# Kernel optimization log

Measured on AMD Instinct MI355X. Metric: run time of the kernel, lower is better.

Reference implementation:

```python
import jax, jax.numpy as jnp
import numpy as np

B, S, H = 2, 2048, 2048
NH = 16
HD = H // NH  # 128


def setup_inputs() -> dict:
    key = jax.random.key(0)
    ks = jax.random.split(key, 6)
    sc = 0.02
    return {
        "x": jax.random.normal(ks[0], (B, S, H), dtype=jnp.float32),
        "attention_mask": jnp.zeros((B, S), dtype=jnp.float32),
        "Wq": jax.random.normal(ks[1], (H, H), dtype=jnp.float32) * sc,
        "bq": jnp.zeros((H,), dtype=jnp.float32),
        "Wk": jax.random.normal(ks[2], (H, H), dtype=jnp.float32) * sc,
        "bk": jnp.zeros((H,), dtype=jnp.float32),
        "Wv": jax.random.normal(ks[3], (H, H), dtype=jnp.float32) * sc,
        "bv": jnp.zeros((H,), dtype=jnp.float32),
        "Wo": jax.random.normal(ks[4], (H, H), dtype=jnp.float32) * sc,
        "bo": jnp.zeros((H,), dtype=jnp.float32),
    }


def reference(x, attention_mask, Wq, bq, Wk, bk, Wv, bv, Wo, bo):
    b, s, h = x.shape
    q = (x @ Wq + bq).reshape(b, s, NH, HD)
    k = (x @ Wk + bk).reshape(b, s, NH, HD)
    v = (x @ Wv + bv).reshape(b, s, NH, HD)
    scale = 1.0 / jnp.sqrt(jnp.asarray(HD, dtype=x.dtype))
    scores = jnp.einsum('bqhd,bkhd->bhqk', q, k) * scale
    scores = scores + attention_mask[:, None, None, :]
    weights = jax.nn.softmax(scores, axis=-1)
    attn = jnp.einsum('bhqk,bkhd->bqhd', weights, v).reshape(b, s, h)
    return attn @ Wo + bo
```

## Files before the change

### kernel.cpp

```cpp
#include <hip/hip_runtime.h>
#include <hip/hip_bf16.h>
#include <stdint.h>

#define BB   2
#define SS   2048
#define HHH  2048
#define NHH  16
#define HDD  128
#define MTOT 4096

typedef __bf16 bf16x8 __attribute__((ext_vector_type(8)));
typedef float  f32x4  __attribute__((ext_vector_type(4)));
typedef float  f32x16 __attribute__((ext_vector_type(16)));

#define MFMA16(a, b, c) __builtin_amdgcn_mfma_f32_16x16x32_bf16((a), (b), (c), 0, 0, 0)
#define MFMA32(a, b, c) __builtin_amdgcn_mfma_f32_32x32x16_bf16((a), (b), (c), 0, 0, 0)

__device__ __forceinline__ unsigned short f2bf(float f) {
    union { float f; unsigned u; } v; v.f = f;
    unsigned r = v.u + 0x7FFFu + ((v.u >> 16) & 1u);
    return (unsigned short)(r >> 16);
}

__device__ __forceinline__ unsigned packbf(float a, float b) {
    union { __bf16 h[2]; unsigned u; } p;
    p.h[0] = (__bf16)a; p.h[1] = (__bf16)b;
    return p.u;
}

__device__ __forceinline__ void pswap(unsigned &a, unsigned &b) {
    asm("v_permlane32_swap_b32 %0, %1" : "+v"(a), "+v"(b));
}

__device__ __forceinline__ float2 xswap(float x) {
    unsigned a = __builtin_bit_cast(unsigned, x);
    unsigned b;
    asm("v_mov_b32 %0, %1" : "=v"(b) : "v"(a));
    asm("v_permlane32_swap_b32 %0, %1" : "+v"(a), "+v"(b));
    return make_float2(__builtin_bit_cast(float, a), __builtin_bit_cast(float, b));
}

__device__ __forceinline__ void gload16(const void* src, void* lds) {
    __builtin_amdgcn_global_load_lds(
        (__attribute__((address_space(1))) void*)src,
        (__attribute__((address_space(3))) void*)lds,
        16, 0, 0);
}

__global__ void cast_f32_bf16(const float* __restrict__ in,
                              unsigned short* __restrict__ out, int n) {
    int i = (blockIdx.x * blockDim.x + threadIdx.x) * 4;
    int stride = gridDim.x * blockDim.x * 4;
    for (; i < n; i += stride) {
        float4 v = *(const float4*)(in + i);
        ushort4 o;
        o.x = f2bf(v.x); o.y = f2bf(v.y); o.z = f2bf(v.z); o.w = f2bf(v.w);
        *(ushort4*)(out + i) = o;
    }
}

__global__ void scale_mask(const float* __restrict__ in, float* __restrict__ out) {
    int i = blockIdx.x * 256 + threadIdx.x;
    out[i] = in[i] * 1.4426950408889634f;
}

__global__ void transpose_cast4(const float* __restrict__ W0, const float* __restrict__ W1,
                                const float* __restrict__ W2, const float* __restrict__ W3,
                                unsigned short* __restrict__ out) {
    const float* in = blockIdx.z == 0 ? W0 : blockIdx.z == 1 ? W1 : blockIdx.z == 2 ? W2 : W3;
    unsigned short* o = out + (size_t)blockIdx.z * ((size_t)HHH * HHH);
    __shared__ float tile[32][33];
    int c0 = blockIdx.x * 32, r0 = blockIdx.y * 32;
    int tx = threadIdx.x, ty = threadIdx.y;
    #pragma unroll
    for (int i = 0; i < 32; i += 8)
        tile[ty + i][tx] = in[(size_t)(r0 + ty + i) * HHH + c0 + tx];
    __syncthreads();
    #pragma unroll
    for (int i = 0; i < 32; i += 8)
        o[(size_t)(c0 + ty + i) * HHH + r0 + tx] = f2bf(tile[tx][ty + i]);
}

template<int MODE>
__global__ __launch_bounds__(512, 2) void gemm8_bf16(
    const unsigned short* __restrict__ A,
    const unsigned short* __restrict__ Bt,
    const float* __restrict__ bias,
    void* __restrict__ Cout,
    int M, int N, int K)
{
    __shared__ __align__(16) unsigned char sm[147456];
    const int tid = threadIdx.x;
    const int wv = tid >> 6, ln = tid & 63;
    const int g = ln >> 4, r = ln & 15;
    const int wr = wv >> 2, wc = wv & 3;

    const int bid = blockIdx.x;
    const int lb = (bid & 7) * 32 + (bid >> 3);
    const int m0 = (lb & 31) * 128;
    const int n0 = (lb >> 5) * 256;

    unsigned srcA[2]; int ldsA[2];
    #pragma unroll
    for (int j = 0; j < 2; ++j) {
        int o = j * 8192 + tid * 16;
        int row = o >> 7;
        int lg = ((o >> 4) & 7) ^ (row & 7);
        srcA[j] = (unsigned)(m0 + row) * K + lg * 8;
        ldsA[j] = o;
    }
    unsigned srcB[4]; int ldsB[4];
    #pragma unroll
    for (int j = 0; j < 4; ++j) {
        int o = j * 8192 + tid * 16;
        int row = o >> 7;
        int lg = ((o >> 4) & 7) ^ (row & 7);
        srcB[j] = (unsigned)(n0 + row) * K + lg * 8;
        ldsB[j] = 16384 + o;
    }

    f32x4 acc[4][4];
    #pragma unroll
    for (int i = 0; i < 4; ++i)
        #pragma unroll
        for (int j = 0; j < 4; ++j)
            acc[i][j] = (f32x4){0.f, 0.f, 0.f, 0.f};

    const int NT = K >> 6;

    {
        unsigned char* b0 = sm;
        unsigned char* b1 = sm + 49152;
        #pragma unroll
        for (int j = 0; j < 2; ++j) gload16(A + srcA[j], b0 + ldsA[j]);
        #pragma unroll
        for (int j = 0; j < 4; ++j) gload16(Bt + srcB[j], b0 + ldsB[j]);
        #pragma unroll
        for (int j = 0; j < 2; ++j) gload16(A + srcA[j] + 64, b1 + ldsA[j]);
        #pragma unroll
        for (int j = 0; j < 4; ++j) gload16(Bt + srcB[j] + 64, b1 + ldsB[j]);
    }
    asm volatile("s_waitcnt vmcnt(6)" ::: "memory");
    __builtin_amdgcn_s_barrier();

    int csel = 0;
    int psel = 2;
    for (int t = 0; t < NT; ++t) {
        const unsigned char* Ab = sm + csel * 49152;
        const unsigned char* Bb = Ab + 16384;
        unsigned char* Pb = sm + psel * 49152;
        const bool pre = (t + 2 < NT);
        const int ko = (t + 2) * 64;

        bf16x8 af[2][2], bfr[4][2];
        #define LDA(mi, ks) (*(const bf16x8*)(Ab + (wr * 64 + (mi) * 16 + r) * 128 + \
                             ((((ks) << 2) + g) ^ ((wr * 64 + (mi) * 16 + r) & 7)) * 16))
        #define LDB(ni, ks) (*(const bf16x8*)(Bb + (wc * 64 + (ni) * 16 + r) * 128 + \
                             ((((ks) << 2) + g) ^ ((wc * 64 + (ni) * 16 + r) & 7)) * 16))

        af[0][0] = LDA(0, 0); af[0][1] = LDA(0, 1);
        af[1][0] = LDA(1, 0); af[1][1] = LDA(1, 1);
        #pragma unroll
        for (int ni = 0; ni < 4; ++ni) {
            bfr[ni][0] = LDB(ni, 0);
            bfr[ni][1] = LDB(ni, 1);
        }
        if (pre) { gload16(Bt + srcB[0] + ko, Pb + ldsB[0]);
                   gload16(Bt + srcB[1] + ko, Pb + ldsB[1]);
                   gload16(Bt + srcB[2] + ko, Pb + ldsB[2]); }
        __builtin_amdgcn_s_barrier();
        asm volatile("s_waitcnt lgkmcnt(0)" ::: "memory");
        __builtin_amdgcn_s_setprio(1);
        #pragma unroll
        for (int mi = 0; mi < 2; ++mi)
            #pragma unroll
            for (int ni = 0; ni < 4; ++ni)
                #pragma unroll
                for (int ks = 0; ks < 2; ++ks)
                    acc[mi][ni] = MFMA16(af[mi][ks], bfr[ni][ks], acc[mi][ni]);
        __builtin_amdgcn_s_setprio(0);
        __builtin_amdgcn_s_barrier();

        af[0][0] = LDA(2, 0); af[0][1] = LDA(2, 1);
        af[1][0] = LDA(3, 0); af[1][1] = LDA(3, 1);
        if (pre) { gload16(Bt + srcB[3] + ko, Pb + ldsB[3]);
                   gload16(A + srcA[0] + ko, Pb + ldsA[0]);
                   gload16(A + srcA[1] + ko, Pb + ldsA[1]); }
        __builtin_amdgcn_s_barrier();
        asm volatile("s_waitcnt lgkmcnt(0)" ::: "memory");
        __builtin_amdgcn_s_setprio(1);
        #pragma unroll
        for (int mi = 0; mi < 2; ++mi)
            #pragma unroll
            for (int ni = 0; ni < 4; ++ni)
                #pragma unroll
                for (int ks = 0; ks < 2; ++ks)
                    acc[mi + 2][ni] = MFMA16(af[mi][ks], bfr[ni][ks], acc[mi + 2][ni]);
        __builtin_amdgcn_s_setprio(0);

        if (pre) asm volatile("s_waitcnt vmcnt(6)" ::: "memory");
        else     asm volatile("s_waitcnt vmcnt(0)" ::: "memory");
        __builtin_amdgcn_s_barrier();

        csel = (csel == 2) ? 0 : csel + 1;
        psel = (psel == 2) ? 0 : psel + 1;
        #undef LDA
        #undef LDB
    }

    #pragma unroll
    for (int mt = 0; mt < 4; ++mt) {
        #pragma unroll
        for (int nt = 0; nt < 4; ++nt) {
            int col = n0 + wc * 64 + nt * 16 + r;
            float bvv = bias[col];
            f32x4 a = acc[mt][nt];
            int mrow = m0 + wr * 64 + mt * 16 + g * 4;
            if (MODE == 0) {
                #pragma unroll
                for (int q = 0; q < 4; ++q)
                    ((unsigned short*)Cout)[(size_t)(mrow + q) * N + col] = f2bf(a[q] + bvv);
            } else if (MODE == 2) {
                #pragma unroll
                for (int q = 0; q < 4; ++q)
                    ((float*)Cout)[(size_t)(mrow + q) * N + col] = a[q] + bvv;
            } else {
                int b = mrow >> 11, s0x = mrow & 2047;
                ushort4 o;
                o.x = f2bf(a[0] + bvv); o.y = f2bf(a[1] + bvv);
                o.z = f2bf(a[2] + bvv); o.w = f2bf(a[3] + bvv);
                *(ushort4*)((unsigned short*)Cout + ((size_t)(b * 2048 + col)) * 2048 + s0x) = o;
            }
        }
    }
}

__global__ __launch_bounds__(256, 2) void attn_fwd(
    const unsigned short* __restrict__ Q,
    const unsigned short* __restrict__ K,
    const unsigned short* __restrict__ V,
    const float* __restrict__ maskl2,
    unsigned short* __restrict__ O)
{
    __shared__ __align__(16) unsigned char sm[57344];
    const int tid = threadIdx.x, wv = tid >> 6, ln = tid & 63;
    const int hi = ln >> 5, qr = ln & 31;

    const int bid = blockIdx.x;
    const int lb = (bid & 7) * 64 + (bid >> 3);
    const int qb = lb & 15;
    const int bh = lb >> 4;
    const int h = bh & 15, b = bh >> 4;

    const size_t rowQ0 = (size_t)(b * 2048 + qb * 128 + wv * 32);
    const float SCL2 = 0.08838834764831845f * 1.4426950408889634f;

    unsigned srcK[2], srcV[2];
    int ldsK[2], ldsV[2];
    #pragma unroll
    for (int i = 0; i < 2; ++i) {
        int ch = wv * 2 + i;
        int o = ch * 1024 + ln * 16;
        { int row = o >> 8; int gl = ((o >> 4) & 15) ^ (row & 7);
          srcK[i] = (unsigned)((b * 2048 + row) * 2048 + h * 128 + gl * 8);
          ldsK[i] = o; }
        { int d = o >> 6; int gl = ((o >> 4) & 3) ^ ((d >> 1) & 3);
          srcV[i] = (unsigned)((b * 2048 + h * 128 + d) * 2048 + gl * 8);
          ldsV[i] = 8192 + o; }
    }

    #define STAGE(t, base) { \
        _Pragma("unroll") \
        for (int i = 0; i < 2; ++i) { \
            gload16(K + srcK[i] + (unsigned)(t) * (32u * 2048u), sm + (base) + ldsK[i]); \
            gload16(V + srcV[i] + (unsigned)(t) * 32u, sm + (base) + ldsV[i]); \
        } }

    #pragma unroll
    for (int i = 0; i < 2; ++i)
        gload16(maskl2 + b * 2048 + wv * 512 + i * 256 + ln * 4,
                sm + 49152 + wv * 2048 + i * 1024);
    STAGE(0, 0); STAGE(1, 16384); STAGE(2, 32768);

    bf16x8 qf[8];
    #pragma unroll
    for (int ks = 0; ks < 8; ++ks)
        qf[ks] = *(const bf16x8*)(Q + (rowQ0 + qr) * 2048 + h * 128 + ks * 16 + hi * 8);

    f32x16 acc[4];
    #pragma unroll
    for (int i = 0; i < 4; ++i)
        #pragma unroll
        for (int j = 0; j < 16; ++j)
            acc[i][j] = 0.f;
    float mr = -3.0e38f, lr = 0.f;

    const float* ml = (const float*)(sm + 49152);

    asm volatile("s_waitcnt vmcnt(8)" ::: "memory");
    __builtin_amdgcn_s_barrier();

    int bufo = 0;
    for (int t = 0; t < 64; ++t) {
        const unsigned char* Kt = sm + bufo;
        const unsigned char* Vt = Kt + 8192;

        f32x4 mk[4];
        #pragma unroll
        for (int rg = 0; rg < 4; ++rg)
            mk[rg] = *(const f32x4*)(ml + t * 32 + rg * 8 + hi * 4);

        f32x16 sfA, sfB;
        #pragma unroll
        for (int j = 0; j < 16; ++j) { sfA[j] = 0.f; sfB[j] = 0.f; }
        __builtin_amdgcn_s_setprio(1);
        #pragma unroll
        for (int ks = 0; ks < 4; ++ks) {
            int s0 = (2 * ks + hi) ^ (qr & 7);
            bf16x8 kf = *(const bf16x8*)(Kt + qr * 256 + s0 * 16);
            sfA = MFMA32(kf, qf[ks], sfA);
        }
        #pragma unroll
        for (int ks = 4; ks < 8; ++ks) {
            int s0 = (2 * ks + hi) ^ (qr & 7);
            bf16x8 kf = *(const bf16x8*)(Kt + qr * 256 + s0 * 16);
            sfB = MFMA32(kf, qf[ks], sfB);
        }
        __builtin_amdgcn_s_setprio(0);

        float sv[16];
        #pragma unroll
        for (int reg = 0; reg < 16; ++reg)
            sv[reg] = (sfA[reg] + sfB[reg]) * SCL2 + mk[reg >> 2][reg & 3];

        float mx[8];
        #pragma unroll
        for (int j = 0; j < 8; ++j)
            mx[j] = fmaxf(sv[2 * j], sv[2 * j + 1]);
        float m01 = fmaxf(fmaxf(fmaxf(mx[0], mx[1]), fmaxf(mx[2], mx[3])),
                          fmaxf(fmaxf(mx[4], mx[5]), fmaxf(mx[6], mx[7])));
        float2 mp = xswap(m01);
        float mt = fmaxf(mp.x, mp.y);

        float alpha = 1.f;
        int allskip = __all(mt <= mr + 8.f);
        if (!allskip) {
            float nm = fmaxf(mr, mt);
            alpha = __builtin_amdgcn_exp2f(mr - nm);
            mr = nm;
            #pragma unroll
            for (int dblk = 0; dblk < 4; ++dblk)
                #pragma unroll
                for (int reg = 0; reg < 16; ++reg)
                    acc[dblk][reg] *= alpha;
        }

        float s0 = 0.f, s1 = 0.f, s2 = 0.f, s3 = 0.f;
        #pragma unroll
        for (int reg = 0; reg < 16; reg += 4) {
            float p0 = __builtin_amdgcn_exp2f(sv[reg + 0] - mr);
            float p1 = __builtin_amdgcn_exp2f(sv[reg + 1] - mr);
            float p2 = __builtin_amdgcn_exp2f(sv[reg + 2] - mr);
            float p3 = __builtin_amdgcn_exp2f(sv[reg + 3] - mr);
            sv[reg + 0] = p0; sv[reg + 1] = p1;
            sv[reg + 2] = p2; sv[reg + 3] = p3;
            s0 += p0; s1 += p1; s2 += p2; s3 += p3;
        }
        float rsl = (s0 + s1) + (s2 + s3);
        float2 rp = xswap(rsl);
        float rs = rp.x + rp.y;
        lr = lr * alpha + rs;

        bf16x8 pfr[2];
        #pragma unroll
        for (int kb16 = 0; kb16 < 2; ++kb16) {
            unsigned W00 = packbf(sv[(2*kb16+0)*4 + 0], sv[(2*kb16+0)*4 + 1]);
            unsigned W01 = packbf(sv[(2*kb16+0)*4 + 2], sv[(2*kb16+0)*4 + 3]);
            unsigned W10 = packbf(sv[(2*kb16+1)*4 + 0], sv[(2*kb16+1)*4 + 1]);
            unsigned W11 = packbf(sv[(2*kb16+1)*4 + 2], sv[(2*kb16+1)*4 + 3]);
            pswap(W00, W10);
            pswap(W01, W11);
            union { unsigned w[4]; bf16x8 v; } u;
            u.w[0] = W00; u.w[1] = W01; u.w[2] = W10; u.w[3] = W11;
            pfr[kb16] = u.v;
        }

        __builtin_amdgcn_s_setprio(1);
        #pragma unroll
        for (int dblk = 0; dblk < 4; ++dblk) {
            int d = dblk * 32 + qr;
            f32x16 a = acc[dblk];
            #pragma unroll
            for (int kb16 = 0; kb16 < 2; ++kb16) {
                int s = (2 * kb16 + hi) ^ ((d >> 1) & 3);
                bf16x8 vf = *(const bf16x8*)(Vt + d * 64 + s * 16);
                a = MFMA32(vf, pfr[kb16], a);
            }
            acc[dblk] = a;
        }
        __builtin_amdgcn_s_setprio(0);

        asm volatile("s_waitcnt vmcnt(4)" ::: "memory");
        __builtin_amdgcn_s_barrier();

        if (t + 3 < 64) STAGE(t + 3, bufo);
        bufo = (bufo == 32768) ? 0 : bufo + 16384;
    }

    float linv = 1.f / lr;
    unsigned short* orow = O + (rowQ0 + qr) * 2048 + h * 128;
    #pragma unroll
    for (int dblk = 0; dblk < 4; ++dblk)
        #pragma unroll
        for (int rg = 0; rg < 4; ++rg) {
            float v0 = acc[dblk][rg * 4 + 0] * linv;
            float v1 = acc[dblk][rg * 4 + 1] * linv;
            float v2 = acc[dblk][rg * 4 + 2] * linv;
            float v3 = acc[dblk][rg * 4 + 3] * linv;
            uint2 o;
            o.x = packbf(v0, v1);
            o.y = packbf(v2, v3);
            *(uint2*)(orow + dblk * 32 + rg * 8 + hi * 4) = o;
        }
    #undef STAGE
}

extern "C" void kernel_launch(void* const* d_in, const int* in_sizes, int n_in,
                              void* d_out, int out_size, void* d_ws, size_t ws_size,
                              hipStream_t stream)
{
    (void)in_sizes; (void)n_in; (void)out_size; (void)ws_size;
    const float* x    = (const float*)d_in[0];
    const float* mask = (const float*)d_in[1];
    const float* Wq   = (const float*)d_in[2];
    const float* bq   = (const float*)d_in[3];
    const float* Wk   = (const float*)d_in[4];
    const float* bk   = (const float*)d_in[5];
    const float* Wv   = (const float*)d_in[6];
    const float* bv   = (const float*)d_in[7];
    const float* Wo   = (const float*)d_in[8];
    const float* bo   = (const float*)d_in[9];
    float* out = (float*)d_out;

    char* ws = (char*)d_ws;
    unsigned short* xb  = (unsigned short*)(ws);
    unsigned short* Wqt = (unsigned short*)(ws + (16u << 20));
    unsigned short* Wkt = (unsigned short*)(ws + (24u << 20));
    unsigned short* Wvt = (unsigned short*)(ws + (32u << 20));
    unsigned short* Wot = (unsigned short*)(ws + (40u << 20));
    unsigned short* Qb  = (unsigned short*)(ws + (48u << 20));
    unsigned short* Kb  = (unsigned short*)(ws + (64u << 20));
    unsigned short* Vtb = (unsigned short*)(ws + (80u << 20));
    unsigned short* Ab  = (unsigned short*)(ws + (16u << 20));
    float*          mkl = (float*)(ws + (32u << 20));

    cast_f32_bf16<<<2048, 256, 0, stream>>>(x, xb, MTOT * HHH);
    transpose_cast4<<<dim3(64, 64, 4), dim3(32, 8), 0, stream>>>(Wq, Wk, Wv, Wo, Wqt);

    gemm8_bf16<0><<<256, 512, 0, stream>>>(xb, Wqt, bq, Qb,  MTOT, HHH, HHH);
    gemm8_bf16<0><<<256, 512, 0, stream>>>(xb, Wkt, bk, Kb,  MTOT, HHH, HHH);
    gemm8_bf16<1><<<256, 512, 0, stream>>>(xb, Wvt, bv, Vtb, MTOT, HHH, HHH);

    scale_mask<<<(BB * SS) / 256, 256, 0, stream>>>(mask, mkl);
    attn_fwd<<<512, 256, 0, stream>>>(Qb, Kb, Vtb, mkl, Ab);

    gemm8_bf16<2><<<256, 512, 0, stream>>>(Ab, Wot, bo, out, MTOT, HHH, HHH);
}
```

Measured before the change: 279.6 us.

## Merge QKV projections into one launch and software-pipeline QK^T in attention

The three Q/K/V projection GEMMs are merged into a single 768-block launch over the concatenated transposed weights, with per-region bias and output-layout selection in the epilogue. This removes two launches and fills the GPU better than three 256-block GEMMs would. The attention kernel is restructured so the QK^T scores for the next key tile are computed before the current tile's softmax/PV step, with a peeled prologue and epilogue and adjusted waitcnt/barriers, so score MFMAs overlap the softmax work. The cost is more live registers, an extra barrier per iteration, and more complex synchronisation.

```diff
diff --git a/kernel.cpp b/kernel.cpp
--- a/kernel.cpp
+++ b/kernel.cpp
@@ -81,13 +81,110 @@
         o[(size_t)(c0 + ty + i) * HHH + r0 + tx] = f2bf(tile[tx][ty + i]);
 }
 
-template<int MODE>
-__global__ __launch_bounds__(512, 2) void gemm8_bf16(
+#define GEMM_CORE(A_, Bt_, K_, m0_, n0_)                                              \
+    unsigned srcA[2]; int ldsA[2];                                                    \
+    _Pragma("unroll")                                                                 \
+    for (int j = 0; j < 2; ++j) {                                                     \
+        int o = j * 8192 + tid * 16;                                                  \
+        int row = o >> 7;                                                             \
+        int lg = ((o >> 4) & 7) ^ (row & 7);                                          \
+        srcA[j] = (unsigned)(m0_ + row) * K_ + lg * 8;                                \
+        ldsA[j] = o;                                                                  \
+    }                                                                                 \
+    unsigned srcB[4]; int ldsB[4];                                                    \
+    _Pragma("unroll")                                                                 \
+    for (int j = 0; j < 4; ++j) {                                                     \
+        int o = j * 8192 + tid * 16;                                                  \
+        int row = o >> 7;                                                             \
+        int lg = ((o >> 4) & 7) ^ (row & 7);                                          \
+        srcB[j] = (unsigned)(n0_ + row) * K_ + lg * 8;                                \
+        ldsB[j] = 16384 + o;                                                          \
+    }                                                                                 \
+    f32x4 acc[4][4];                                                                  \
+    _Pragma("unroll")                                                                 \
+    for (int i = 0; i < 4; ++i)                                                       \
+        _Pragma("unroll")                                                             \
+        for (int j = 0; j < 4; ++j)                                                   \
+            acc[i][j] = (f32x4){0.f, 0.f, 0.f, 0.f};                                  \
+    const int NT = K_ >> 6;                                                           \
+    {                                                                                 \
+        unsigned char* b0 = sm;                                                       \
+        unsigned char* b1 = sm + 49152;                                               \
+        _Pragma("unroll")                                                             \
+        for (int j = 0; j < 2; ++j) gload16(A_ + srcA[j], b0 + ldsA[j]);              \
+        _Pragma("unroll")                                                             \
+        for (int j = 0; j < 4; ++j) gload16(Bt_ + srcB[j], b0 + ldsB[j]);             \
+        _Pragma("unroll")                                                             \
+        for (int j = 0; j < 2; ++j) gload16(A_ + srcA[j] + 64, b1 + ldsA[j]);         \
+        _Pragma("unroll")                                                             \
+        for (int j = 0; j < 4; ++j) gload16(Bt_ + srcB[j] + 64, b1 + ldsB[j]);        \
+    }                                                                                 \
+    asm volatile("s_waitcnt vmcnt(6)" ::: "memory");                                  \
+    __builtin_amdgcn_s_barrier();                                                     \
+    int csel = 0, psel = 2;                                                           \
+    for (int t = 0; t < NT; ++t) {                                                    \
+        const unsigned char* Ab = sm + csel * 49152;                                  \
+        const unsigned char* Bb = Ab + 16384;                                         \
+        unsigned char* Pb = sm + psel * 49152;                                        \
+        const bool pre = (t + 2 < NT);                                                \
+        const int ko = (t + 2) * 64;                                                  \
+        bf16x8 af[2][2], bfr[4][2];                                                   \
+        af[0][0] = LDA(0, 0); af[0][1] = LDA(0, 1);                                   \
+        af[1][0] = LDA(1, 0); af[1][1] = LDA(1, 1);                                   \
+        _Pragma("unroll")                                                             \
+        for (int ni = 0; ni < 4; ++ni) { bfr[ni][0] = LDB(ni, 0); bfr[ni][1] = LDB(ni, 1); } \
+        if (pre) { gload16(Bt_ + srcB[0] + ko, Pb + ldsB[0]);                         \
+                   gload16(Bt_ + srcB[1] + ko, Pb + ldsB[1]);                         \
+                   gload16(Bt_ + srcB[2] + ko, Pb + ldsB[2]); }                       \
+        __builtin_amdgcn_s_barrier();                                                 \
+        asm volatile("s_waitcnt lgkmcnt(0)" ::: "memory");                            \
+        __builtin_amdgcn_s_setprio(1);                                                \
+        _Pragma("unroll")                                                             \
+        for (int mi = 0; mi < 2; ++mi)                                                \
+            _Pragma("unroll")                                                         \
+            for (int ni = 0; ni < 4; ++ni)                                            \
+                _Pragma("unroll")                                                     \
+                for (int ks = 0; ks < 2; ++ks)                                        \
+                    acc[mi][ni] = MFMA16(af[mi][ks], bfr[ni][ks], acc[mi][ni]);       \
+        __builtin_amdgcn_s_setprio(0);                                                \
+        __builtin_amdgcn_s_barrier();                                                 \
+        af[0][0] = LDA(2, 0); af[0][1] = LDA(2, 1);                                   \
+        af[1][0] = LDA(3, 0); af[1][1] = LDA(3, 1);                                   \
+        if (pre) { gload16(Bt_ + srcB[3] + ko, Pb + ldsB[3]);                         \
+                   gload16(A_ + srcA[0] + ko, Pb + ldsA[0]);                          \
+                   gload16(A_ + srcA[1] + ko, Pb + ldsA[1]); }                        \
+        __builtin_amdgcn_s_barrier();                                                 \
+        asm volatile("s_waitcnt lgkmcnt(0)" ::: "memory");                            \
+        __builtin_amdgcn_s_setprio(1);                                                \
+        _Pragma("unroll")                                                             \
+        for (int mi = 0; mi < 2; ++mi)                                                \
+            _Pragma("unroll")                                                         \
+            for (int ni = 0; ni < 4; ++ni)                                            \
+                _Pragma("unroll")                                                     \
+                for (int ks = 0; ks < 2; ++ks)                                        \
+                    acc[mi + 2][ni] = MFMA16(af[mi][ks], bfr[ni][ks], acc[mi + 2][ni]); \
+        __builtin_amdgcn_s_setprio(0);                                                \
+        if (pre) asm volatile("s_waitcnt vmcnt(6)" ::: "memory");                     \
+        else     asm volatile("s_waitcnt vmcnt(0)" ::: "memory");                     \
+        __builtin_amdgcn_s_barrier();                                                 \
+        csel = (csel == 2) ? 0 : csel + 1;                                            \
+        psel = (psel == 2) ? 0 : psel + 1;                                            \
+    }
+
+#define LDA(mi, ks) (*(const bf16x8*)(Ab + (wr * 64 + (mi) * 16 + r) * 128 + \
+                     ((((ks) << 2) + g) ^ ((wr * 64 + (mi) * 16 + r) & 7)) * 16))
+#define LDB(ni, ks) (*(const bf16x8*)(Bb + (wc * 64 + (ni) * 16 + r) * 128 + \
+                     ((((ks) << 2) + g) ^ ((wc * 64 + (ni) * 16 + r) & 7)) * 16))
+
+__global__ __launch_bounds__(512, 2) void gemmQKV(
     const unsigned short* __restrict__ A,
     const unsigned short* __restrict__ Bt,
-    const float* __restrict__ bias,
-    void* __restrict__ Cout,
-    int M, int N, int K)
+    const float* __restrict__ bq,
+    const float* __restrict__ bk,
+    const float* __restrict__ bv,
+    unsigned short* __restrict__ Qb,
+    unsigned short* __restrict__ Kb,
+    unsigned short* __restrict__ Vtb)
 {
     __shared__ __align__(16) unsigned char sm[147456];
     const int tid = threadIdx.x;
@@ -96,117 +193,59 @@
     const int wr = wv >> 2, wc = wv & 3;
 
     const int bid = blockIdx.x;
+    const int lb = (bid & 7) * 96 + (bid >> 3);
+    const int m0 = (lb & 31) * 128;
+    const int n0 = (lb >> 5) * 256;
+    const int K = HHH;
+
+    GEMM_CORE(A, Bt, K, m0, n0)
+
+    const int region = n0 >> 11;
+    const float* bp = region == 0 ? bq : (region == 1 ? bk : bv);
+    unsigned short* outp = region == 0 ? Qb : Kb;
+    #pragma unroll
+    for (int mt = 0; mt < 4; ++mt) {
+        #pragma unroll
+        for (int nt = 0; nt < 4; ++nt) {
+            int col = n0 + wc * 64 + nt * 16 + r;
+            int lcol = col & 2047;
+            float bvv = bp[lcol];
+            f32x4 a = acc[mt][nt];
+            int mrow = m0 + wr * 64 + mt * 16 + g * 4;
+            if (region < 2) {
+                #pragma unroll
+                for (int q = 0; q < 4; ++q)
+                    outp[(size_t)(mrow + q) * 2048 + lcol] = f2bf(a[q] + bvv);
+            } else {
+                int b = mrow >> 11, s0x = mrow & 2047;
+                ushort4 o;
+                o.x = f2bf(a[0] + bvv); o.y = f2bf(a[1] + bvv);
+                o.z = f2bf(a[2] + bvv); o.w = f2bf(a[3] + bvv);
+                *(ushort4*)(Vtb + ((size_t)(b * 2048 + lcol)) * 2048 + s0x) = o;
+            }
+        }
+    }
+}
+
+__global__ __launch_bounds__(512, 2) void gemmO(
+    const unsigned short* __restrict__ A,
+    const unsigned short* __restrict__ Bt,
+    const float* __restrict__ bias,
+    float* __restrict__ Cout)
+{
+    __shared__ __align__(16) unsigned char sm[147456];
+    const int tid = threadIdx.x;
+    const int wv = tid >> 6, ln = tid & 63;
+    const int g = ln >> 4, r = ln & 15;
+    const int wr = wv >> 2, wc = wv & 3;
+
+    const int bid = blockIdx.x;
     const int lb = (bid & 7) * 32 + (bid >> 3);
     const int m0 = (lb & 31) * 128;
     const int n0 = (lb >> 5) * 256;
-
-    unsigned srcA[2]; int ldsA[2];
-    #pragma unroll
-    for (int j = 0; j < 2; ++j) {
-        int o = j * 8192 + tid * 16;
-        int row = o >> 7;
-        int lg = ((o >> 4) & 7) ^ (row & 7);
-        srcA[j] = (unsigned)(m0 + row) * K + lg * 8;
-        ldsA[j] = o;
-    }
-    unsigned srcB[4]; int ldsB[4];
-    #pragma unroll
-    for (int j = 0; j < 4; ++j) {
-        int o = j * 8192 + tid * 16;
-        int row = o >> 7;
-        int lg = ((o >> 4) & 7) ^ (row & 7);
-        srcB[j] = (unsigned)(n0 + row) * K + lg * 8;
-        ldsB[j] = 16384 + o;
-    }
-
-    f32x4 acc[4][4];
-    #pragma unroll
-    for (int i = 0; i < 4; ++i)
-        #pragma unroll
-        for (int j = 0; j < 4; ++j)
-            acc[i][j] = (f32x4){0.f, 0.f, 0.f, 0.f};
-
-    const int NT = K >> 6;
-
-    {
-        unsigned char* b0 = sm;
-        unsigned char* b1 = sm + 49152;
-        #pragma unroll
-        for (int j = 0; j < 2; ++j) gload16(A + srcA[j], b0 + ldsA[j]);
-        #pragma unroll
-        for (int j = 0; j < 4; ++j) gload16(Bt + srcB[j], b0 + ldsB[j]);
-        #pragma unroll
-        for (int j = 0; j < 2; ++j) gload16(A + srcA[j] + 64, b1 + ldsA[j]);
-        #pragma unroll
-        for (int j = 0; j < 4; ++j) gload16(Bt + srcB[j] + 64, b1 + ldsB[j]);
-    }
-    asm volatile("s_waitcnt vmcnt(6)" ::: "memory");
-    __builtin_amdgcn_s_barrier();
-
-    int csel = 0;
-    int psel = 2;
-    for (int t = 0; t < NT; ++t) {
-        const unsigned char* Ab = sm + csel * 49152;
-        const unsigned char* Bb = Ab + 16384;
-        unsigned char* Pb = sm + psel * 49152;
-        const bool pre = (t + 2 < NT);
-        const int ko = (t + 2) * 64;
-
-        bf16x8 af[2][2], bfr[4][2];
-        #define LDA(mi, ks) (*(const bf16x8*)(Ab + (wr * 64 + (mi) * 16 + r) * 128 + \
-                             ((((ks) << 2) + g) ^ ((wr * 64 + (mi) * 16 + r) & 7)) * 16))
-        #define LDB(ni, ks) (*(const bf16x8*)(Bb + (wc * 64 + (ni) * 16 + r) * 128 + \
-                             ((((ks) << 2) + g) ^ ((wc * 64 + (ni) * 16 + r) & 7)) * 16))
-
-        af[0][0] = LDA(0, 0); af[0][1] = LDA(0, 1);
-        af[1][0] = LDA(1, 0); af[1][1] = LDA(1, 1);
-        #pragma unroll
-        for (int ni = 0; ni < 4; ++ni) {
-            bfr[ni][0] = LDB(ni, 0);
-            bfr[ni][1] = LDB(ni, 1);
-        }
-        if (pre) { gload16(Bt + srcB[0] + ko, Pb + ldsB[0]);
-                   gload16(Bt + srcB[1] + ko, Pb + ldsB[1]);
-                   gload16(Bt + srcB[2] + ko, Pb + ldsB[2]); }
-        __builtin_amdgcn_s_barrier();
-        asm volatile("s_waitcnt lgkmcnt(0)" ::: "memory");
-        __builtin_amdgcn_s_setprio(1);
-        #pragma unroll
-        for (int mi = 0; mi < 2; ++mi)
-            #pragma unroll
-            for (int ni = 0; ni < 4; ++ni)
-                #pragma unroll
-                for (int ks = 0; ks < 2; ++ks)
-                    acc[mi][ni] = MFMA16(af[mi][ks], bfr[ni][ks], acc[mi][ni]);
-        __builtin_amdgcn_s_setprio(0);
-        __builtin_amdgcn_s_barrier();
-
-        af[0][0] = LDA(2, 0); af[0][1] = LDA(2, 1);
-        af[1][0] = LDA(3, 0); af[1][1] = LDA(3, 1);
-        if (pre) { gload16(Bt + srcB[3] + ko, Pb + ldsB[3]);
-                   gload16(A + srcA[0] + ko, Pb + ldsA[0]);
-                   gload16(A + srcA[1] + ko, Pb + ldsA[1]); }
-        __builtin_amdgcn_s_barrier();
-        asm volatile("s_waitcnt lgkmcnt(0)" ::: "memory");
-        __builtin_amdgcn_s_setprio(1);
-        #pragma unroll
-        for (int mi = 0; mi < 2; ++mi)
-            #pragma unroll
-            for (int ni = 0; ni < 4; ++ni)
-                #pragma unroll
-                for (int ks = 0; ks < 2; ++ks)
-                    acc[mi + 2][ni] = MFMA16(af[mi][ks], bfr[ni][ks], acc[mi + 2][ni]);
-        __builtin_amdgcn_s_setprio(0);
-
-        if (pre) asm volatile("s_waitcnt vmcnt(6)" ::: "memory");
-        else     asm volatile("s_waitcnt vmcnt(0)" ::: "memory");
-        __builtin_amdgcn_s_barrier();
-
-        csel = (csel == 2) ? 0 : csel + 1;
-        psel = (psel == 2) ? 0 : psel + 1;
-        #undef LDA
-        #undef LDB
-    }
+    const int K = HHH;
+
+    GEMM_CORE(A, Bt, K, m0, n0)
 
     #pragma unroll
     for (int mt = 0; mt < 4; ++mt) {
@@ -216,24 +255,15 @@
             float bvv = bias[col];
             f32x4 a = acc[mt][nt];
             int mrow = m0 + wr * 64 + mt * 16 + g * 4;
-            if (MODE == 0) {
-                #pragma unroll
-                for (int q = 0; q < 4; ++q)
-                    ((unsigned short*)Cout)[(size_t)(mrow + q) * N + col] = f2bf(a[q] + bvv);
-            } else if (MODE == 2) {
-                #pragma unroll
-                for (int q = 0; q < 4; ++q)
-                    ((float*)Cout)[(size_t)(mrow + q) * N + col] = a[q] + bvv;
-            } else {
-                int b = mrow >> 11, s0x = mrow & 2047;
-                ushort4 o;
-                o.x = f2bf(a[0] + bvv); o.y = f2bf(a[1] + bvv);
-                o.z = f2bf(a[2] + bvv); o.w = f2bf(a[3] + bvv);
-                *(ushort4*)((unsigned short*)Cout + ((size_t)(b * 2048 + col)) * 2048 + s0x) = o;
-            }
-        }
-    }
-}
+            #pragma unroll
+            for (int q = 0; q < 4; ++q)
+                Cout[(size_t)(mrow + q) * 2048 + col] = a[q] + bvv;
+        }
+    }
+}
+
+#undef LDA
+#undef LDB
 
 __global__ __launch_bounds__(256, 2) void attn_fwd(
     const unsigned short* __restrict__ Q,
@@ -255,6 +285,11 @@
     const size_t rowQ0 = (size_t)(b * 2048 + qb * 128 + wv * 32);
     const float SCL2 = 0.08838834764831845f * 1.4426950408889634f;
 
+    bf16x8 qf[8];
+    #pragma unroll
+    for (int ks = 0; ks < 8; ++ks)
+        qf[ks] = *(const bf16x8*)(Q + (rowQ0 + qr) * 2048 + h * 128 + ks * 16 + hi * 8);
+
     unsigned srcK[2], srcV[2];
     int ldsK[2], ldsV[2];
     #pragma unroll
@@ -282,11 +317,6 @@
                 sm + 49152 + wv * 2048 + i * 1024);
     STAGE(0, 0); STAGE(1, 16384); STAGE(2, 32768);
 
-    bf16x8 qf[8];
-    #pragma unroll
-    for (int ks = 0; ks < 8; ++ks)
-        qf[ks] = *(const bf16x8*)(Q + (rowQ0 + qr) * 2048 + h * 128 + ks * 16 + hi * 8);
-
     f32x16 acc[4];
     #pragma unroll
     for (int i = 0; i < 4; ++i)
@@ -297,18 +327,36 @@
 
     const float* ml = (const float*)(sm + 49152);
 
-    asm volatile("s_waitcnt vmcnt(8)" ::: "memory");
+    asm volatile("s_waitcnt vmcnt(4)" ::: "memory");
     __builtin_amdgcn_s_barrier();
 
-    int bufo = 0;
-    for (int t = 0; t < 64; ++t) {
-        const unsigned char* Kt = sm + bufo;
-        const unsigned char* Vt = Kt + 8192;
-
-        f32x4 mk[4];
-        #pragma unroll
-        for (int rg = 0; rg < 4; ++rg)
-            mk[rg] = *(const f32x4*)(ml + t * 32 + rg * 8 + hi * 4);
+    float sv[16];
+    {
+        f32x16 sfA, sfB;
+        #pragma unroll
+        for (int j = 0; j < 16; ++j) { sfA[j] = 0.f; sfB[j] = 0.f; }
+        #pragma unroll
+        for (int ks = 0; ks < 4; ++ks) {
+            int s0 = (2 * ks + hi) ^ (qr & 7);
+            bf16x8 kf = *(const bf16x8*)(sm + qr * 256 + s0 * 16);
+            sfA = MFMA32(kf, qf[ks], sfA);
+        }
+        #pragma unroll
+        for (int ks = 4; ks < 8; ++ks) {
+            int s0 = (2 * ks + hi) ^ (qr & 7);
+            bf16x8 kf = *(const bf16x8*)(sm + qr * 256 + s0 * 16);
+            sfB = MFMA32(kf, qf[ks], sfB);
+        }
+        #pragma unroll
+        for (int reg = 0; reg < 16; ++reg)
+            sv[reg] = (sfA[reg] + sfB[reg]) * SCL2 + ml[(reg >> 2) * 8 + hi * 4 + (reg & 3)];
+    }
+
+    int base0 = 0;
+    for (int t = 0; t < 63; ++t) {
+        const int baseN = (base0 == 32768) ? 0 : base0 + 16384;
+        const unsigned char* Vt = sm + base0 + 8192;
+        const unsigned char* Kn = sm + baseN;
 
         f32x16 sfA, sfB;
         #pragma unroll
@@ -317,21 +365,16 @@
         #pragma unroll
         for (int ks = 0; ks < 4; ++ks) {
             int s0 = (2 * ks + hi) ^ (qr & 7);
-            bf16x8 kf = *(const bf16x8*)(Kt + qr * 256 + s0 * 16);
+            bf16x8 kf = *(const bf16x8*)(Kn + qr * 256 + s0 * 16);
             sfA = MFMA32(kf, qf[ks], sfA);
         }
         #pragma unroll
         for (int ks = 4; ks < 8; ++ks) {
             int s0 = (2 * ks + hi) ^ (qr & 7);
-            bf16x8 kf = *(const bf16x8*)(Kt + qr * 256 + s0 * 16);
+            bf16x8 kf = *(const bf16x8*)(Kn + qr * 256 + s0 * 16);
             sfB = MFMA32(kf, qf[ks], sfB);
         }
         __builtin_amdgcn_s_setprio(0);
-
-        float sv[16];
-        #pragma unroll
-        for (int reg = 0; reg < 16; ++reg)
-            sv[reg] = (sfA[reg] + sfB[reg]) * SCL2 + mk[reg >> 2][reg & 3];
 
         float mx[8];
         #pragma unroll
@@ -385,6 +428,11 @@
             pfr[kb16] = u.v;
         }
 
+        #pragma unroll
+        for (int reg = 0; reg < 16; ++reg)
+            sv[reg] = (sfA[reg] + sfB[reg]) * SCL2
+                      + ml[(t + 1) * 32 + (reg >> 2) * 8 + hi * 4 + (reg & 3)];
+
         __builtin_amdgcn_s_setprio(1);
         #pragma unroll
         for (int dblk = 0; dblk < 4; ++dblk) {
@@ -400,11 +448,82 @@
         }
         __builtin_amdgcn_s_setprio(0);
 
-        asm volatile("s_waitcnt vmcnt(4)" ::: "memory");
         __builtin_amdgcn_s_barrier();
-
-        if (t + 3 < 64) STAGE(t + 3, bufo);
-        bufo = (bufo == 32768) ? 0 : bufo + 16384;
+        if (t + 3 < 64) {
+            STAGE(t + 3, base0);
+            asm volatile("s_waitcnt vmcnt(4)" ::: "memory");
+        } else {
+            asm volatile("s_waitcnt vmcnt(0)" ::: "memory");
+        }
+        __builtin_amdgcn_s_barrier();
+        base0 = baseN;
+    }
+
+    {
+        const unsigned char* Vt = sm + base0 + 8192;
+        float mx[8];
+        #pragma unroll
+        for (int j = 0; j < 8; ++j)
+            mx[j] = fmaxf(sv[2 * j], sv[2 * j + 1]);
+        float m01 = fmaxf(fmaxf(fmaxf(mx[0], mx[1]), fmaxf(mx[2], mx[3])),
+                          fmaxf(fmaxf(mx[4], mx[5]), fmaxf(mx[6], mx[7])));
+        float2 mp = xswap(m01);
+        float mt = fmaxf(mp.x, mp.y);
+
+        float alpha = 1.f;
+        int allskip = __all(mt <= mr + 8.f);
+        if (!allskip) {
+            float nm = fmaxf(mr, mt);
+            alpha = __builtin_amdgcn_exp2f(mr - nm);
+            mr = nm;
+            #pragma unroll
+            for (int dblk = 0; dblk < 4; ++dblk)
+                #pragma unroll
+                for (int reg = 0; reg < 16; ++reg)
+                    acc[dblk][reg] *= alpha;
+        }
+
+        float s0 = 0.f, s1 = 0.f, s2 = 0.f, s3 = 0.f;
+        #pragma unroll
+        for (int reg = 0; reg < 16; reg += 4) {
+            float p0 = __builtin_amdgcn_exp2f(sv[reg + 0] - mr);
+            float p1 = __builtin_amdgcn_exp2f(sv[reg + 1] - mr);
+            float p2 = __builtin_amdgcn_exp2f(sv[reg + 2] - mr);
+            float p3 = __builtin_amdgcn_exp2f(sv[reg + 3] - mr);
+            sv[reg + 0] = p0; sv[reg + 1] = p1;
+            sv[reg + 2] = p2; sv[reg + 3] = p3;
+            s0 += p0; s1 += p1; s2 += p2; s3 += p3;
+        }
+        float rsl = (s0 + s1) + (s2 + s3);
+        float2 rp = xswap(rsl);
+        lr = lr * alpha + rp.x + rp.y;
+
+        bf16x8 pfr[2];
+        #pragma unroll
+        for (int kb16 = 0; kb16 < 2; ++kb16) {
+            unsigned W00 = packbf(sv[(2*kb16+0)*4 + 0], sv[(2*kb16+0)*4 + 1]);
+            unsigned W01 = packbf(sv[(2*kb16+0)*4 + 2], sv[(2*kb16+0)*4 + 3]);
+            unsigned W10 = packbf(sv[(2*kb16+1)*4 + 0], sv[(2*kb16+1)*4 + 1]);
+            unsigned W11 = packbf(sv[(2*kb16+1)*4 + 2], sv[(2*kb16+1)*4 + 3]);
+            pswap(W00, W10);
+            pswap(W01, W11);
+            union { unsigned w[4]; bf16x8 v; } u;
+            u.w[0] = W00; u.w[1] = W01; u.w[2] = W10; u.w[3] = W11;
+            pfr[kb16] = u.v;
+        }
+
+        #pragma unroll
+        for (int dblk = 0; dblk < 4; ++dblk) {
+            int d = dblk * 32 + qr;
+            f32x16 a = acc[dblk];
+            #pragma unroll
+            for (int kb16 = 0; kb16 < 2; ++kb16) {
+                int s = (2 * kb16 + hi) ^ ((d >> 1) & 3);
+                bf16x8 vf = *(const bf16x8*)(Vt + d * 64 + s * 16);
+                a = MFMA32(vf, pfr[kb16], a);
+            }
+            acc[dblk] = a;
+        }
     }
 
     float linv = 1.f / lr;
@@ -445,8 +564,6 @@
     char* ws = (char*)d_ws;
     unsigned short* xb  = (unsigned short*)(ws);
     unsigned short* Wqt = (unsigned short*)(ws + (16u << 20));
-    unsigned short* Wkt = (unsigned short*)(ws + (24u << 20));
-    unsigned short* Wvt = (unsigned short*)(ws + (32u << 20));
     unsigned short* Wot = (unsigned short*)(ws + (40u << 20));
     unsigned short* Qb  = (unsigned short*)(ws + (48u << 20));
     unsigned short* Kb  = (unsigned short*)(ws + (64u << 20));
@@ -457,12 +574,10 @@
     cast_f32_bf16<<<2048, 256, 0, stream>>>(x, xb, MTOT * HHH);
     transpose_cast4<<<dim3(64, 64, 4), dim3(32, 8), 0, stream>>>(Wq, Wk, Wv, Wo, Wqt);
 
-    gemm8_bf16<0><<<256, 512, 0, stream>>>(xb, Wqt, bq, Qb,  MTOT, HHH, HHH);
-    gemm8_bf16<0><<<256, 512, 0, stream>>>(xb, Wkt, bk, Kb,  MTOT, HHH, HHH);
-    gemm8_bf16<1><<<256, 512, 0, stream>>>(xb, Wvt, bv, Vtb, MTOT, HHH, HHH);
+    gemmQKV<<<768, 512, 0, stream>>>(xb, Wqt, bq, bk, bv, Qb, Kb, Vtb);
 
     scale_mask<<<(BB * SS) / 256, 256, 0, stream>>>(mask, mkl);
     attn_fwd<<<512, 256, 0, stream>>>(Qb, Kb, Vtb, mkl, Ab);
 
-    gemm8_bf16<2><<<256, 512, 0, stream>>>(Ab, Wot, bo, out, MTOT, HHH, HHH);
-}
+    gemmO<<<256, 512, 0, stream>>>(Ab, Wot, bo, out);
+}
```

Result: no change. 275.8 us (-1.4%).

## Fuse QKV projections into one 256x256-tile GEMM and software-pipeline attention QK

Applied to the files above, without the earlier changes.

Replaces the three separate Q/K/V projection launches with one GEMM over the concatenated transposed weights. It uses larger 256x256 tiles with double-buffered LDS staging, and picks the bias and output layout per N region. In attention, Q fragments are loaded before the K/V staging, and the QK^T scores for the next tile are computed while the current tile's PV product runs, with a peeled final iteration. This is meant to cut launch overhead, raise reuse per tile and overlap softmax/QK work with PV. The cost is higher register pressure and a 2-stage instead of 3-stage GEMM pipeline.

```diff
diff --git a/kernel.cpp b/kernel.cpp
--- a/kernel.cpp
+++ b/kernel.cpp
@@ -81,19 +81,143 @@
         o[(size_t)(c0 + ty + i) * HHH + r0 + tx] = f2bf(tile[tx][ty + i]);
 }
 
-template<int MODE>
-__global__ __launch_bounds__(512, 2) void gemm8_bf16(
+__global__ __launch_bounds__(512, 2) void gemmQKV(
+    const unsigned short* __restrict__ A,
+    const unsigned short* __restrict__ Bt,
+    const float* __restrict__ bq,
+    const float* __restrict__ bk,
+    const float* __restrict__ bv,
+    unsigned short* __restrict__ Qb,
+    unsigned short* __restrict__ Kb,
+    unsigned short* __restrict__ Vtb)
+{
+    __shared__ __align__(16) unsigned char sm[131072];
+    const int tid = threadIdx.x;
+    const int wv = tid >> 6, ln = tid & 63;
+    const int g = ln >> 4, r = ln & 15;
+    const int wr = wv >> 2, wc = wv & 3;
+    const int K = HHH;
+
+    const int bid = blockIdx.x;
+    const int lb = (bid & 7) * 48 + (bid >> 3);
+    const int m0 = (lb & 15) * 256;
+    const int n0 = (lb >> 4) * 256;
+
+    unsigned srcA[4], srcB[4];
+    int ldsA[4], ldsB[4];
+    #pragma unroll
+    for (int j = 0; j < 4; ++j) {
+        int o = j * 8192 + tid * 16;
+        int row = o >> 7;
+        int lg = ((o >> 4) & 7) ^ (row & 7);
+        srcA[j] = (unsigned)(m0 + row) * K + lg * 8;
+        srcB[j] = (unsigned)(n0 + row) * K + lg * 8;
+        ldsA[j] = o;
+        ldsB[j] = 32768 + o;
+    }
+
+    #define STG(t, base) { \
+        _Pragma("unroll") \
+        for (int j = 0; j < 4; ++j) gload16(A + srcA[j] + (t) * 64, sm + (base) + ldsA[j]); \
+        _Pragma("unroll") \
+        for (int j = 0; j < 4; ++j) gload16(Bt + srcB[j] + (t) * 64, sm + (base) + ldsB[j]); \
+    }
+
+    f32x4 acc[8][4];
+    #pragma unroll
+    for (int i = 0; i < 8; ++i)
+        #pragma unroll
+        for (int j = 0; j < 4; ++j)
+            acc[i][j] = (f32x4){0.f, 0.f, 0.f, 0.f};
+
+    STG(0, 0); STG(1, 65536);
+    asm volatile("s_waitcnt vmcnt(8)" ::: "memory");
+    __builtin_amdgcn_s_barrier();
+
+    #define LDA(mi, kk) (*(const bf16x8*)(Ab + (wr * 128 + (mi) * 16 + r) * 128 + \
+                         ((((kk) << 2) + g) ^ ((wr * 128 + (mi) * 16 + r) & 7)) * 16))
+    #define LDB(ni, kk) (*(const bf16x8*)(Bb + (wc * 64 + (ni) * 16 + r) * 128 + \
+                         ((((kk) << 2) + g) ^ ((wc * 64 + (ni) * 16 + r) & 7)) * 16))
+
+    for (int t = 0; t < 32; ++t) {
+        const unsigned char* Ab = sm + (t & 1) * 65536;
+        const unsigned char* Bb = Ab + 32768;
+
+        bf16x8 bfr[4][2];
+        #pragma unroll
+        for (int ni = 0; ni < 4; ++ni) {
+            bfr[ni][0] = LDB(ni, 0);
+            bfr[ni][1] = LDB(ni, 1);
+        }
+
+        #pragma unroll
+        for (int p = 0; p < 4; ++p) {
+            bf16x8 af[2][2];
+            af[0][0] = LDA(2 * p, 0);     af[0][1] = LDA(2 * p, 1);
+            af[1][0] = LDA(2 * p + 1, 0); af[1][1] = LDA(2 * p + 1, 1);
+            __builtin_amdgcn_s_setprio(1);
+            #pragma unroll
+            for (int mi = 0; mi < 2; ++mi)
+                #pragma unroll
+                for (int ni = 0; ni < 4; ++ni)
+                    #pragma unroll
+                    for (int kk = 0; kk < 2; ++kk)
+                        acc[2 * p + mi][ni] = MFMA16(af[mi][kk], bfr[ni][kk], acc[2 * p + mi][ni]);
+            __builtin_amdgcn_s_setprio(0);
+        }
+
+        __builtin_amdgcn_s_barrier();
+        if (t + 2 < 32) {
+            STG(t + 2, (t & 1) * 65536);
+            asm volatile("s_waitcnt vmcnt(8)" ::: "memory");
+        } else {
+            asm volatile("s_waitcnt vmcnt(0)" ::: "memory");
+        }
+        __builtin_amdgcn_s_barrier();
+    }
+    #undef LDA
+    #undef LDB
+    #undef STG
+
+    const int region = n0 >> 11;
+    const float* bp = region == 0 ? bq : (region == 1 ? bk : bv);
+    unsigned short* outp = region == 0 ? Qb : Kb;
+    #pragma unroll
+    for (int mt = 0; mt < 8; ++mt) {
+        #pragma unroll
+        for (int nt = 0; nt < 4; ++nt) {
+            int col = n0 + wc * 64 + nt * 16 + r;
+            int lcol = col & 2047;
+            float bvv = bp[lcol];
+            f32x4 a = acc[mt][nt];
+            int mrow = m0 + wr * 128 + mt * 16 + g * 4;
+            if (region < 2) {
+                #pragma unroll
+                for (int q = 0; q < 4; ++q)
+                    outp[(size_t)(mrow + q) * 2048 + lcol] = f2bf(a[q] + bvv);
+            } else {
+                int b = mrow >> 11, s0x = mrow & 2047;
+                ushort4 o;
+                o.x = f2bf(a[0] + bvv); o.y = f2bf(a[1] + bvv);
+                o.z = f2bf(a[2] + bvv); o.w = f2bf(a[3] + bvv);
+                *(ushort4*)(Vtb + ((size_t)(b * 2048 + lcol)) * 2048 + s0x) = o;
+            }
+        }
+    }
+}
+
+__global__ __launch_bounds__(512, 2) void gemmO(
     const unsigned short* __restrict__ A,
     const unsigned short* __restrict__ Bt,
     const float* __restrict__ bias,
-    void* __restrict__ Cout,
-    int M, int N, int K)
+    float* __restrict__ Cout)
 {
     __shared__ __align__(16) unsigned char sm[147456];
     const int tid = threadIdx.x;
     const int wv = tid >> 6, ln = tid & 63;
     const int g = ln >> 4, r = ln & 15;
     const int wr = wv >> 2, wc = wv & 3;
+    const int K = HHH;
 
     const int bid = blockIdx.x;
     const int lb = (bid & 7) * 32 + (bid >> 3);
@@ -143,8 +267,12 @@
     asm volatile("s_waitcnt vmcnt(6)" ::: "memory");
     __builtin_amdgcn_s_barrier();
 
-    int csel = 0;
-    int psel = 2;
+    #define LDA(mi, ks) (*(const bf16x8*)(Ab + (wr * 64 + (mi) * 16 + r) * 128 + \
+                         ((((ks) << 2) + g) ^ ((wr * 64 + (mi) * 16 + r) & 7)) * 16))
+    #define LDB(ni, ks) (*(const bf16x8*)(Bb + (wc * 64 + (ni) * 16 + r) * 128 + \
+                         ((((ks) << 2) + g) ^ ((wc * 64 + (ni) * 16 + r) & 7)) * 16))
+
+    int csel = 0, psel = 2;
     for (int t = 0; t < NT; ++t) {
         const unsigned char* Ab = sm + csel * 49152;
         const unsigned char* Bb = Ab + 16384;
@@ -153,18 +281,10 @@
         const int ko = (t + 2) * 64;
 
         bf16x8 af[2][2], bfr[4][2];
-        #define LDA(mi, ks) (*(const bf16x8*)(Ab + (wr * 64 + (mi) * 16 + r) * 128 + \
-                             ((((ks) << 2) + g) ^ ((wr * 64 + (mi) * 16 + r) & 7)) * 16))
-        #define LDB(ni, ks) (*(const bf16x8*)(Bb + (wc * 64 + (ni) * 16 + r) * 128 + \
-                             ((((ks) << 2) + g) ^ ((wc * 64 + (ni) * 16 + r) & 7)) * 16))
-
         af[0][0] = LDA(0, 0); af[0][1] = LDA(0, 1);
         af[1][0] = LDA(1, 0); af[1][1] = LDA(1, 1);
         #pragma unroll
-        for (int ni = 0; ni < 4; ++ni) {
-            bfr[ni][0] = LDB(ni, 0);
-            bfr[ni][1] = LDB(ni, 1);
-        }
+        for (int ni = 0; ni < 4; ++ni) { bfr[ni][0] = LDB(ni, 0); bfr[ni][1] = LDB(ni, 1); }
         if (pre) { gload16(Bt + srcB[0] + ko, Pb + ldsB[0]);
                    gload16(Bt + srcB[1] + ko, Pb + ldsB[1]);
                    gload16(Bt + srcB[2] + ko, Pb + ldsB[2]); }
@@ -204,9 +324,9 @@
 
         csel = (csel == 2) ? 0 : csel + 1;
         psel = (psel == 2) ? 0 : psel + 1;
-        #undef LDA
-        #undef LDB
-    }
+    }
+    #undef LDA
+    #undef LDB
 
     #pragma unroll
     for (int mt = 0; mt < 4; ++mt) {
@@ -216,21 +336,9 @@
             float bvv = bias[col];
             f32x4 a = acc[mt][nt];
             int mrow = m0 + wr * 64 + mt * 16 + g * 4;
-            if (MODE == 0) {
-                #pragma unroll
-                for (int q = 0; q < 4; ++q)
-                    ((unsigned short*)Cout)[(size_t)(mrow + q) * N + col] = f2bf(a[q] + bvv);
-            } else if (MODE == 2) {
-                #pragma unroll
-                for (int q = 0; q < 4; ++q)
-                    ((float*)Cout)[(size_t)(mrow + q) * N + col] = a[q] + bvv;
-            } else {
-                int b = mrow >> 11, s0x = mrow & 2047;
-                ushort4 o;
-                o.x = f2bf(a[0] + bvv); o.y = f2bf(a[1] + bvv);
-                o.z = f2bf(a[2] + bvv); o.w = f2bf(a[3] + bvv);
-                *(ushort4*)((unsigned short*)Cout + ((size_t)(b * 2048 + col)) * 2048 + s0x) = o;
-            }
+            #pragma unroll
+            for (int q = 0; q < 4; ++q)
+                Cout[(size_t)(mrow + q) * 2048 + col] = a[q] + bvv;
         }
     }
 }
@@ -255,6 +363,11 @@
     const size_t rowQ0 = (size_t)(b * 2048 + qb * 128 + wv * 32);
     const float SCL2 = 0.08838834764831845f * 1.4426950408889634f;
 
+    bf16x8 qf[8];
+    #pragma unroll
+    for (int ks = 0; ks < 8; ++ks)
+        qf[ks] = *(const bf16x8*)(Q + (rowQ0 + qr) * 2048 + h * 128 + ks * 16 + hi * 8);
+
     unsigned srcK[2], srcV[2];
     int ldsK[2], ldsV[2];
     #pragma unroll
@@ -282,11 +395,6 @@
                 sm + 49152 + wv * 2048 + i * 1024);
     STAGE(0, 0); STAGE(1, 16384); STAGE(2, 32768);
 
-    bf16x8 qf[8];
-    #pragma unroll
-    for (int ks = 0; ks < 8; ++ks)
-        qf[ks] = *(const bf16x8*)(Q + (rowQ0 + qr) * 2048 + h * 128 + ks * 16 + hi * 8);
-
     f32x16 acc[4];
     #pragma unroll
     for (int i = 0; i < 4; ++i)
@@ -297,18 +405,36 @@
 
     const float* ml = (const float*)(sm + 49152);
 
-    asm volatile("s_waitcnt vmcnt(8)" ::: "memory");
+    asm volatile("s_waitcnt vmcnt(4)" ::: "memory");
     __builtin_amdgcn_s_barrier();
 
-    int bufo = 0;
-    for (int t = 0; t < 64; ++t) {
-        const unsigned char* Kt = sm + bufo;
-        const unsigned char* Vt = Kt + 8192;
-
-        f32x4 mk[4];
-        #pragma unroll
-        for (int rg = 0; rg < 4; ++rg)
-            mk[rg] = *(const f32x4*)(ml + t * 32 + rg * 8 + hi * 4);
+    float sv[16];
+    {
+        f32x16 sfA, sfB;
+        #pragma unroll
+        for (int j = 0; j < 16; ++j) { sfA[j] = 0.f; sfB[j] = 0.f; }
+        #pragma unroll
+        for (int ks = 0; ks < 4; ++ks) {
+            int s0 = (2 * ks + hi) ^ (qr & 7);
+            bf16x8 kf = *(const bf16x8*)(sm + qr * 256 + s0 * 16);
+            sfA = MFMA32(kf, qf[ks], sfA);
+        }
+        #pragma unroll
+        for (int ks = 4; ks < 8; ++ks) {
+            int s0 = (2 * ks + hi) ^ (qr & 7);
+            bf16x8 kf = *(const bf16x8*)(sm + qr * 256 + s0 * 16);
+            sfB = MFMA32(kf, qf[ks], sfB);
+        }
+        #pragma unroll
+        for (int reg = 0; reg < 16; ++reg)
+            sv[reg] = (sfA[reg] + sfB[reg]) * SCL2 + ml[(reg >> 2) * 8 + hi * 4 + (reg & 3)];
+    }
+
+    int base0 = 0;
+    for (int t = 0; t < 63; ++t) {
+        const int baseN = (base0 == 32768) ? 0 : base0 + 16384;
+        const unsigned char* Vt = sm + base0 + 8192;
+        const unsigned char* Kn = sm + baseN;
 
         f32x16 sfA, sfB;
         #pragma unroll
@@ -317,21 +443,16 @@
         #pragma unroll
         for (int ks = 0; ks < 4; ++ks) {
             int s0 = (2 * ks + hi) ^ (qr & 7);
-            bf16x8 kf = *(const bf16x8*)(Kt + qr * 256 + s0 * 16);
+            bf16x8 kf = *(const bf16x8*)(Kn + qr * 256 + s0 * 16);
             sfA = MFMA32(kf, qf[ks], sfA);
         }
         #pragma unroll
         for (int ks = 4; ks < 8; ++ks) {
             int s0 = (2 * ks + hi) ^ (qr & 7);
-            bf16x8 kf = *(const bf16x8*)(Kt + qr * 256 + s0 * 16);
+            bf16x8 kf = *(const bf16x8*)(Kn + qr * 256 + s0 * 16);
             sfB = MFMA32(kf, qf[ks], sfB);
         }
         __builtin_amdgcn_s_setprio(0);
-
-        float sv[16];
-        #pragma unroll
-        for (int reg = 0; reg < 16; ++reg)
-            sv[reg] = (sfA[reg] + sfB[reg]) * SCL2 + mk[reg >> 2][reg & 3];
 
         float mx[8];
         #pragma unroll
@@ -385,6 +506,11 @@
             pfr[kb16] = u.v;
         }
 
+        #pragma unroll
+        for (int reg = 0; reg < 16; ++reg)
+            sv[reg] = (sfA[reg] + sfB[reg]) * SCL2
+                      + ml[(t + 1) * 32 + (reg >> 2) * 8 + hi * 4 + (reg & 3)];
+
         __builtin_amdgcn_s_setprio(1);
         #pragma unroll
         for (int dblk = 0; dblk < 4; ++dblk) {
@@ -400,11 +526,82 @@
         }
         __builtin_amdgcn_s_setprio(0);
 
-        asm volatile("s_waitcnt vmcnt(4)" ::: "memory");
-        __builtin_amdgcn_s_barrier();
-
-        if (t + 3 < 64) STAGE(t + 3, bufo);
-        bufo = (bufo == 32768) ? 0 : bufo + 16384;
+        __builtin_amdgcn_s_barrier();
+        if (t + 3 < 64) {
+            STAGE(t + 3, base0);
+            asm volatile("s_waitcnt vmcnt(4)" ::: "memory");
+        } else {
+            asm volatile("s_waitcnt vmcnt(0)" ::: "memory");
+        }
+        __builtin_amdgcn_s_barrier();
+        base0 = baseN;
+    }
+
+    {
+        const unsigned char* Vt = sm + base0 + 8192;
+        float mx[8];
+        #pragma unroll
+        for (int j = 0; j < 8; ++j)
+            mx[j] = fmaxf(sv[2 * j], sv[2 * j + 1]);
+        float m01 = fmaxf(fmaxf(fmaxf(mx[0], mx[1]), fmaxf(mx[2], mx[3])),
+                          fmaxf(fmaxf(mx[4], mx[5]), fmaxf(mx[6], mx[7])));
+        float2 mp = xswap(m01);
+        float mt = fmaxf(mp.x, mp.y);
+
+        float alpha = 1.f;
+        int allskip = __all(mt <= mr + 8.f);
+        if (!allskip) {
+            float nm = fmaxf(mr, mt);
+            alpha = __builtin_amdgcn_exp2f(mr - nm);
+            mr = nm;
+            #pragma unroll
+            for (int dblk = 0; dblk < 4; ++dblk)
+                #pragma unroll
+                for (int reg = 0; reg < 16; ++reg)
+                    acc[dblk][reg] *= alpha;
+        }
+
+        float s0 = 0.f, s1 = 0.f, s2 = 0.f, s3 = 0.f;
+        #pragma unroll
+        for (int reg = 0; reg < 16; reg += 4) {
+            float p0 = __builtin_amdgcn_exp2f(sv[reg + 0] - mr);
+            float p1 = __builtin_amdgcn_exp2f(sv[reg + 1] - mr);
+            float p2 = __builtin_amdgcn_exp2f(sv[reg + 2] - mr);
+            float p3 = __builtin_amdgcn_exp2f(sv[reg + 3] - mr);
+            sv[reg + 0] = p0; sv[reg + 1] = p1;
+            sv[reg + 2] = p2; sv[reg + 3] = p3;
+            s0 += p0; s1 += p1; s2 += p2; s3 += p3;
+        }
+        float rsl = (s0 + s1) + (s2 + s3);
+        float2 rp = xswap(rsl);
+        lr = lr * alpha + rp.x + rp.y;
+
+        bf16x8 pfr[2];
+        #pragma unroll
+        for (int kb16 = 0; kb16 < 2; ++kb16) {
+            unsigned W00 = packbf(sv[(2*kb16+0)*4 + 0], sv[(2*kb16+0)*4 + 1]);
+            unsigned W01 = packbf(sv[(2*kb16+0)*4 + 2], sv[(2*kb16+0)*4 + 3]);
+            unsigned W10 = packbf(sv[(2*kb16+1)*4 + 0], sv[(2*kb16+1)*4 + 1]);
+            unsigned W11 = packbf(sv[(2*kb16+1)*4 + 2], sv[(2*kb16+1)*4 + 3]);
+            pswap(W00, W10);
+            pswap(W01, W11);
+            union { unsigned w[4]; bf16x8 v; } u;
+            u.w[0] = W00; u.w[1] = W01; u.w[2] = W10; u.w[3] = W11;
+            pfr[kb16] = u.v;
+        }
+
+        #pragma unroll
+        for (int dblk = 0; dblk < 4; ++dblk) {
+            int d = dblk * 32 + qr;
+            f32x16 a = acc[dblk];
+            #pragma unroll
+            for (int kb16 = 0; kb16 < 2; ++kb16) {
+                int s = (2 * kb16 + hi) ^ ((d >> 1) & 3);
+                bf16x8 vf = *(const bf16x8*)(Vt + d * 64 + s * 16);
+                a = MFMA32(vf, pfr[kb16], a);
+            }
+            acc[dblk] = a;
+        }
     }
 
     float linv = 1.f / lr;
@@ -445,8 +642,6 @@
     char* ws = (char*)d_ws;
     unsigned short* xb  = (unsigned short*)(ws);
     unsigned short* Wqt = (unsigned short*)(ws + (16u << 20));
-    unsigned short* Wkt = (unsigned short*)(ws + (24u << 20));
-    unsigned short* Wvt = (unsigned short*)(ws + (32u << 20));
     unsigned short* Wot = (unsigned short*)(ws + (40u << 20));
     unsigned short* Qb  = (unsigned short*)(ws + (48u << 20));
     unsigned short* Kb  = (unsigned short*)(ws + (64u << 20));
@@ -457,12 +652,10 @@
     cast_f32_bf16<<<2048, 256, 0, stream>>>(x, xb, MTOT * HHH);
     transpose_cast4<<<dim3(64, 64, 4), dim3(32, 8), 0, stream>>>(Wq, Wk, Wv, Wo, Wqt);
 
-    gemm8_bf16<0><<<256, 512, 0, stream>>>(xb, Wqt, bq, Qb,  MTOT, HHH, HHH);
-    gemm8_bf16<0><<<256, 512, 0, stream>>>(xb, Wkt, bk, Kb,  MTOT, HHH, HHH);
-    gemm8_bf16<1><<<256, 512, 0, stream>>>(xb, Wvt, bv, Vtb, MTOT, HHH, HHH);
+    gemmQKV<<<384, 512, 0, stream>>>(xb, Wqt, bq, bk, bv, Qb, Kb, Vtb);
 
     scale_mask<<<(BB * SS) / 256, 256, 0, stream>>>(mask, mkl);
     attn_fwd<<<512, 256, 0, stream>>>(Qb, Kb, Vtb, mkl, Ab);
 
-    gemm8_bf16<2><<<256, 512, 0, stream>>>(Ab, Wot, bo, out, MTOT, HHH, HHH);
-}
+    gemmO<<<256, 512, 0, stream>>>(Ab, Wot, bo, out);
+}
```

Result: no change. 285.2 us (+2.0%).
